# Kernel tuning notes

Measured on AMD Instinct MI355X. Metric: run time of the kernel, lower is better.

Reference implementation:

```python
import jax, jax.numpy as jnp
import numpy as np

N = 20000   # nodes
E = 40000   # edges
B = 1000    # graphs
F = 32      # num_features
D = 64      # dim


def setup_inputs() -> dict:
    key = jax.random.key(0)
    ks = jax.random.split(key, 16)
    def g(k, shape, scale=0.05):
        return jax.random.normal(k, shape, jnp.float32) * scale
    return dict(
        x=jax.random.normal(ks[0], (N, F), jnp.float32),
        edge_attr=jax.random.uniform(ks[1], (E, 5), jnp.float32),
        edge_index=jax.random.randint(ks[2], (2, E), 0, N),
        batch=jnp.sort(jax.random.randint(ks[3], (N,), 0, B)),
        W0=g(ks[4], (D, F)), b0=jnp.zeros((D,), jnp.float32),
        We1=g(ks[5], (128, 5)), be1=jnp.zeros((128,), jnp.float32),
        We2=g(ks[6], (D * D, 128), 0.01), be2=jnp.zeros((D * D,), jnp.float32),
        b_conv=jnp.zeros((D,), jnp.float32),
        W_ih=g(ks[7], (3 * D, D)), W_hh=g(ks[8], (3 * D, D)),
        b_ih=jnp.zeros((3 * D,), jnp.float32), b_hh=jnp.zeros((3 * D,), jnp.float32),
        W_ihl=g(ks[9], (4 * D, 2 * D)), W_hhl=g(ks[10], (4 * D, D)),
        b_ihl=jnp.zeros((4 * D,), jnp.float32), b_hhl=jnp.zeros((4 * D,), jnp.float32),
        W1=g(ks[11], (D, 2 * D)), b1=jnp.zeros((D,), jnp.float32),
        W2=g(ks[12], (1, D)), b2=jnp.zeros((1,), jnp.float32),
    )


def reference(x, edge_attr, edge_index, batch, W0, b0, We1, be1, We2, be2,
              b_conv, W_ih, W_hh, b_ih, b_hh, W_ihl, W_hhl, b_ihl, b_hhl,
              W1, b1, W2, b2):
    src, dst = edge_index[0], edge_index[1]
    # lin0 + relu
    out = jax.nn.relu(x @ W0.T + b0)            # [N, D]
    h = out                                     # GRU hidden
    # edge-conditioned weights (identical each iteration in the original)
    We = jax.nn.relu(edge_attr @ We1.T + be1) @ We2.T + be2
    We = We.reshape(E, D, D)                    # [E, in, out]
    deg = jnp.maximum(jax.ops.segment_sum(jnp.ones((E,), out.dtype), dst, N), 1.0)[:, None]
    for _ in range(3):
        msg = jnp.einsum('ei,eio->eo', out[src], We)          # [E, D]
        agg = jax.ops.segment_sum(msg, dst, num_segments=N) / deg
        m = jax.nn.relu(agg + b_conv)
        # GRU cell (gate order r, z, n as in torch)
        gi = m @ W_ih.T + b_ih
        gh = h @ W_hh.T + b_hh
        ir, iz, inn = jnp.split(gi, 3, -1)
        hr, hz, hn = jnp.split(gh, 3, -1)
        r = jax.nn.sigmoid(ir + hr)
        z = jax.nn.sigmoid(iz + hz)
        n = jnp.tanh(inn + r * hn)
        h = (1.0 - z) * n + z * h
        out = h
    # Set2Set pooling (3 processing steps), LSTM gate order i, f, g, o
    q_star = jnp.zeros((B, 2 * D), out.dtype)
    hl = jnp.zeros((B, D), out.dtype)
    cl = jnp.zeros((B, D), out.dtype)
    for _ in range(3):
        gates = q_star @ W_ihl.T + b_ihl + hl @ W_hhl.T + b_hhl
        i_, f_, g_, o_ = jnp.split(gates, 4, -1)
        cl = jax.nn.sigmoid(f_) * cl + jax.nn.sigmoid(i_) * jnp.tanh(g_)
        hl = jax.nn.sigmoid(o_) * jnp.tanh(cl)
        q = hl                                               # [B, D]
        e = jnp.sum(out * q[batch], -1)                      # [N]
        emax = jax.ops.segment_max(e, batch, num_segments=B)
        a = jnp.exp(e - emax[batch])
        a = a / jax.ops.segment_sum(a, batch, num_segments=B)[batch]
        r_ = jax.ops.segment_sum(a[:, None] * out, batch, num_segments=B)
        q_star = jnp.concatenate([q, r_], -1)                # [B, 2D]
    y = jax.nn.relu(q_star @ W1.T + b1)
    pred = (y @ W2.T + b2).reshape(-1)                       # [B]
    return pred
```

## Files before the change

kernel.cpp:

```cpp
#include <hip/hip_runtime.h>

#define NN 20000
#define NE 40000
#define NGR 1000
#define KH 2
#define WTF_BIAS 524288

typedef unsigned short u16;
typedef u16 u16x8 __attribute__((ext_vector_type(8)));
typedef __bf16 bf16x8 __attribute__((ext_vector_type(8)));
typedef float f32x4 __attribute__((ext_vector_type(4)));

union U8 { u16x8 u; bf16x8 b; };

__device__ __forceinline__ u16 f2bf(float f) {
    union { float f; unsigned u; } v; v.f = f;
    unsigned r = v.u + 0x7FFF + ((v.u >> 16) & 1);
    return (u16)(r >> 16);
}
__device__ __forceinline__ float bf2f(u16 h) {
    union { unsigned u; float f; } v; v.u = ((unsigned)h) << 16;
    return v.f;
}
__device__ __forceinline__ float sigmoidf(float x) { return 1.f / (1.f + __expf(-x)); }

__global__ __launch_bounds__(256) void k_cnt(const int* __restrict__ ei, int* __restrict__ cnt)
{
    for (int e = blockIdx.x * 256 + threadIdx.x; e < NE; e += gridDim.x * 256)
        atomicAdd(&cnt[ei[NE + e]], 1);
}

__global__ __launch_bounds__(1024) void k_scan(const int* __restrict__ cnt,
                                               int* __restrict__ rowptr)
{
    __shared__ int ps[1024];
    int t = threadIdx.x;
    int base = t * 20;
    int loc[20];
    int s = 0;
#pragma unroll
    for (int i = 0; i < 20; ++i) {
        int idx = base + i;
        loc[i] = s;
        s += (idx < NN) ? cnt[idx] : 0;
    }
    ps[t] = s;
    __syncthreads();
    for (int off = 1; off < 1024; off <<= 1) {
        int v = (t >= off) ? ps[t - off] : 0;
        __syncthreads();
        ps[t] += v;
        __syncthreads();
    }
    int ex = (t > 0) ? ps[t - 1] : 0;
#pragma unroll
    for (int i = 0; i < 20; ++i) {
        int idx = base + i;
        if (idx < NN) rowptr[idx] = ex + loc[i];
    }
    if (t == 1023) rowptr[NN] = ps[1023];
}

__global__ __launch_bounds__(256) void k_scatter(const int* __restrict__ ei,
    const int* __restrict__ rowptr, int* __restrict__ cur,
    int* __restrict__ epos, int* __restrict__ srcs)
{
    for (int e = blockIdx.x * 256 + threadIdx.x; e < NE; e += gridDim.x * 256) {
        int d = ei[NE + e];
        int pos = rowptr[d] + atomicAdd(&cur[d], 1);
        epos[e] = pos;
        srcs[pos] = ei[e];
    }
}

__global__ __launch_bounds__(256) void k_pre(
    const float* __restrict__ x, const float* __restrict__ ea,
    const int* __restrict__ batch, const int* __restrict__ epos,
    const float* __restrict__ W0, const float* __restrict__ b0,
    const float* __restrict__ We1, const float* __restrict__ be1,
    const float* __restrict__ We2, const float* __restrict__ be2,
    const float* __restrict__ W_ih, const float* __restrict__ W_hh,
    const float* __restrict__ W_ihl, const float* __restrict__ W_hhl,
    const float* __restrict__ W1,
    float* __restrict__ h, u16* __restrict__ outb, u16* __restrict__ h1,
    u16* __restrict__ WtF, int* __restrict__ gstart, int* __restrict__ gend,
    u16* __restrict__ WgF,
    float* __restrict__ WTihl, float* __restrict__ WThhl, float* __restrict__ WT1)
{
    const int b = blockIdx.x;
    const int t = threadIdx.x;

    if (b < 64) {
        for (int idx = b * 256 + t; idx < 90112; idx += 64 * 256) {
            int i = idx;
            if (i < 32768) {
                int j = i & 7, lane = (i >> 3) & 63;
                int nt = (i >> 9) & 15, ks = i >> 13;
                int o = nt * 16 + (lane & 15);
                int k = ks * 32 + (lane >> 4) * 8 + j;
                float v;
                if (o < 128)      v = (k < 64) ? W_ih[o * 64 + k] : W_hh[o * 64 + k - 64];
                else if (o < 192) v = (k < 64) ? W_ih[o * 64 + k] : 0.f;
                else              v = (k >= 64) ? W_hh[(o - 64) * 64 + k - 64] : 0.f;
                WgF[i] = f2bf(v);
                continue;
            }
            i -= 32768;
            if (i < 32768) { WTihl[i] = W_ihl[(i % 256) * 128 + i / 256]; continue; }
            i -= 32768;
            if (i < 16384) { WThhl[i] = W_hhl[(i % 256) * 64 + i / 256]; continue; }
            i -= 16384;
            WT1[i] = W1[(i % 64) * 128 + i / 64];
        }
        return;
    }
    if (b < 320) {
        int wv = (b - 64) * 4 + (t >> 6);
        int lane = t & 63;
        float w0r[32];
#pragma unroll
        for (int f = 0; f < 32; ++f) w0r[f] = W0[lane * 32 + f];
        float b0v = b0[lane];
        for (int n = wv; n < NN; n += 1024) {
            float xv = (lane < 32) ? x[n * 32 + lane] : 0.f;
            float acc = b0v;
#pragma unroll
            for (int f = 0; f < 32; ++f) acc += __shfl(xv, f, 64) * w0r[f];
            float rv = fmaxf(acc, 0.f);
            h[n * 64 + lane] = rv;
            outb[n * 64 + lane] = f2bf(rv);
        }
        return;
    }
    if (b < 832) {
        for (int idx = (b - 320) * 256 + t; idx < NE * 128; idx += 512 * 256) {
            int e = idx >> 7, k = idx & 127;
            float acc = be1[k];
#pragma unroll
            for (int j = 0; j < 5; ++j)
                acc += ea[e * 5 + j] * We1[k * 5 + j];
            h1[(size_t)epos[e] * 128 + k] = f2bf(fmaxf(acc, 0.f));
        }
        return;
    }
    if (b < 960) {
        for (int idx = (b - 832) * 256 + t; idx < WTF_BIAS + 4096; idx += 128 * 256) {
            float v;
            if (idx < WTF_BIAS) {
                int j = idx & 7, lane = (idx >> 3) & 63;
                int nt = (idx >> 9) & 3, s4 = (idx >> 11) & 3, ch = idx >> 13;
                int o = nt * 16 + (lane & 15);
                int k = s4 * 32 + (lane >> 4) * 8 + j;
                v = We2[(size_t)(ch * 64 + o) * 128 + k];
            } else {
                int bx = idx - WTF_BIAS;
                int j = bx & 7, lane = (bx >> 3) & 63;
                int nt = (bx >> 9) & 3, sb = bx >> 11;
                int o = nt * 16 + (lane & 15);
                int i = sb * 32 + (lane >> 4) * 8 + j;
                v = be2[i * 64 + o];
            }
            WtF[idx] = f2bf(v);
        }
        return;
    }
    {
        for (int idx = (b - 960) * 256 + t; idx < NN; idx += 32 * 256) {
            int bg = batch[idx];
            if (idx == 0 || batch[idx - 1] != bg) gstart[bg] = idx;
            if (idx == NN - 1 || batch[idx + 1] != bg) gend[bg] = idx + 1;
        }
    }
}

__global__ __launch_bounds__(256, 3) void k_msg(
    const u16* __restrict__ outb, const u16* __restrict__ h1,
    const u16* __restrict__ WtF, const int* __restrict__ srcs,
    u16* __restrict__ pbuf)
{
    __shared__ __align__(8) u16 svT[64 * 132];
    const int t = threadIdx.x;
    const int eb0 = blockIdx.x * 128;
    const int kh = blockIdx.y;
    const int ohc = (int)blockIdx.z * 2;

#pragma unroll
    for (int r = 0; r < 4; ++r) {
        int cid = t + 256 * r;
        int row = cid >> 3, c8 = cid & 7;
        int e = eb0 + row;
        u16x8 v = {};
        if (e < NE) { int s = srcs[e]; v = *(const u16x8*)(outb + (size_t)s * 64 + c8 * 8); }
        int rs = row ^ (c8 << 2);
#pragma unroll
        for (int j = 0; j < 8; ++j)
            svT[(c8 * 8 + j) * 132 + rs] = v[j];
    }

    const int lane = t & 63, w = t >> 6, r16 = lane & 15, q = lane >> 4;
    const int w32 = w * 32;

    u16x8 h1r[2][4];
#pragma unroll
    for (int sub = 0; sub < 2; ++sub) {
        int e = eb0 + w32 + sub * 16 + r16;
        if (e >= NE) e = NE - 1;
        const u16* hp = h1 + (size_t)e * 128 + q * 8;
#pragma unroll
        for (int s4 = 0; s4 < 4; ++s4)
            h1r[sub][s4] = *(const u16x8*)(hp + s4 * 32);
    }

    f32x4 acc[2][2];
    const f32x4 z4 = {0.f, 0.f, 0.f, 0.f};
#pragma unroll
    for (int sub = 0; sub < 2; ++sub)
#pragma unroll
        for (int nt = 0; nt < 2; ++nt) acc[sub][nt] = z4;

    f32x4 P0[2][2], P1[2][2];
    U8 bufA[8], bufB[8];
    auto LDC = [&](U8 (&dst)[8], int ch) {
        const u16* p = WtF + (size_t)ch * 8192 + ohc * 512 + lane * 8;
#pragma unroll
        for (int s4 = 0; s4 < 4; ++s4)
#pragma unroll
            for (int nt = 0; nt < 2; ++nt)
                dst[s4 * 2 + nt].u = *(const u16x8*)(p + s4 * 2048 + nt * 512);
    };
    auto MF = [&](f32x4 (&P)[2][2], U8 (&bv)[8]) {
#pragma unroll
        for (int s4 = 0; s4 < 4; ++s4)
#pragma unroll
            for (int sub = 0; sub < 2; ++sub) {
                U8 a; a.u = h1r[sub][s4];
#pragma unroll
                for (int nt = 0; nt < 2; ++nt)
                    P[sub][nt] = __builtin_amdgcn_mfma_f32_16x16x32_bf16(
                        a.b, bv[s4 * 2 + nt].b, (s4 == 0) ? z4 : P[sub][nt], 0, 0, 0);
            }
    };
    auto SCALE = [&](f32x4 (&P)[2][2], int ch) {
        int swz = ((ch >> 3) & 7) << 2;
#pragma unroll
        for (int sub = 0; sub < 2; ++sub) {
            int mb = (w32 + sub * 16 + q * 4) ^ swz;
            uint2 rv = *(const uint2*)&svT[ch * 132 + mb];
            union { unsigned u; float f; } c0, c1, c2, c3;
            c0.u = rv.x << 16; c1.u = rv.x & 0xffff0000u;
            c2.u = rv.y << 16; c3.u = rv.y & 0xffff0000u;
#pragma unroll
            for (int nt = 0; nt < 2; ++nt) {
                acc[sub][nt][0] += c0.f * P[sub][nt][0];
                acc[sub][nt][1] += c1.f * P[sub][nt][1];
                acc[sub][nt][2] += c2.f * P[sub][nt][2];
                acc[sub][nt][3] += c3.f * P[sub][nt][3];
            }
        }
    };

    LDC(bufA, kh * 32);
    __syncthreads();
    LDC(bufB, kh * 32 + 1);
    MF(P0, bufA);

#pragma unroll 1
    for (int cc = 0; cc < 30; cc += 2) {
        const int ch = kh * 32 + cc;
        LDC(bufA, ch + 2);
        MF(P1, bufB);
        SCALE(P0, ch);
        LDC(bufB, ch + 3);
        MF(P0, bufA);
        SCALE(P1, ch + 1);
    }
    MF(P1, bufB);
    SCALE(P0, kh * 32 + 30);
    SCALE(P1, kh * 32 + 31);

    if (kh == KH - 1) {
        U8 bvb[2][2];
#pragma unroll
        for (int sb = 0; sb < 2; ++sb)
#pragma unroll
            for (int nt = 0; nt < 2; ++nt)
                bvb[sb][nt].u = *(const u16x8*)(WtF + WTF_BIAS +
                                                ((sb * 4 + ohc + nt) * 64 + lane) * 8);
#pragma unroll
        for (int sub = 0; sub < 2; ++sub) {
            int m = w32 + sub * 16 + r16;
#pragma unroll
            for (int sb = 0; sb < 2; ++sb) {
                U8 a;
#pragma unroll
                for (int j = 0; j < 8; ++j) {
                    int ch = sb * 32 + q * 8 + j;
                    a.u[j] = svT[ch * 132 + (m ^ (((ch >> 3) & 7) << 2))];
                }
#pragma unroll
                for (int nt = 0; nt < 2; ++nt)
                    acc[sub][nt] = __builtin_amdgcn_mfma_f32_16x16x32_bf16(
                        a.b, bvb[sb][nt].b, acc[sub][nt], 0, 0, 0);
            }
        }
    }

#pragma unroll
    for (int sub = 0; sub < 2; ++sub) {
#pragma unroll
        for (int r = 0; r < 4; ++r) {
            int e = eb0 + w32 + sub * 16 + q * 4 + r;
            if (e >= NE) continue;
            u16* pp = pbuf + (size_t)e * (KH * 64) + kh * 64 + r16;
#pragma unroll
            for (int nt = 0; nt < 2; ++nt)
                pp[(ohc + nt) * 16] = f2bf(acc[sub][nt][r]);
        }
    }
}

__global__ __launch_bounds__(256) void k_gru(float* __restrict__ h, u16* __restrict__ outb,
    const u16* __restrict__ pbuf, const int* __restrict__ rowptr,
    const float* __restrict__ b_conv, const u16* __restrict__ WgF,
    const float* __restrict__ b_ih, const float* __restrict__ b_hh)
{
    __shared__ __align__(16) u16 zA[64 * 132];
    __shared__ float hS[64 * 65];
    const int t = threadIdx.x;
    const int lane = t & 63, w = t >> 6, r16 = lane & 15, q = lane >> 4;
    const int n0 = blockIdx.x * 64;
    const int w16 = w * 16;
    float bcv = b_conv[lane];

#pragma unroll 1
    for (int p = 0; p < 16; ++p) {
        int n = n0 + w16 + p;
        float m = 0.f, hvv = 0.f;
        if (n < NN) {
            int rs = rowptr[n], re = rowptr[n + 1];
            float v = 0.f;
            const u16* pb = pbuf + (size_t)rs * (KH * 64);
            for (int j = rs; j < re; ++j) {
                v += bf2f(pb[lane]) + bf2f(pb[64 + lane]);
                pb += KH * 64;
            }
            m = fmaxf(v / fmaxf((float)(re - rs), 1.f) + bcv, 0.f);
            hvv = h[n * 64 + lane];
        }
        zA[(w16 + p) * 132 + lane] = f2bf(m);
        zA[(w16 + p) * 132 + 64 + lane] = f2bf(hvv);
        hS[(w16 + p) * 65 + lane] = hvv;
    }

    u16x8 afr[4];
#pragma unroll
    for (int ks = 0; ks < 4; ++ks)
        afr[ks] = *(const u16x8*)&zA[(w16 + r16) * 132 + ks * 32 + q * 8];

    f32x4 acc[16];
    const f32x4 z4 = {0.f, 0.f, 0.f, 0.f};
#pragma unroll
    for (int nt = 0; nt < 16; ++nt) acc[nt] = z4;

    U8 bA[4], bB[4];
    auto LDB = [&](U8* dst, int nt) {
#pragma unroll
        for (int ks = 0; ks < 4; ++ks)
            dst[ks].u = *(const u16x8*)(WgF + ((ks * 16 + nt) * 64 + lane) * 8);
    };
    LDB(bA, 0);
#pragma unroll
    for (int nt = 0; nt < 16; ++nt) {
        U8* cur = (nt & 1) ? bB : bA;
        U8* nxt = (nt & 1) ? bA : bB;
        if (nt < 15) LDB(nxt, nt + 1);
        f32x4 c = acc[nt];
#pragma unroll
        for (int ks = 0; ks < 4; ++ks) {
            U8 a; a.u = afr[ks];
            c = __builtin_amdgcn_mfma_f32_16x16x32_bf16(a.b, cur[ks].b, c, 0, 0, 0);
        }
        acc[nt] = c;
    }

#pragma unroll
    for (int reg = 0; reg < 4; ++reg) {
        int nl = w16 + q * 4 + reg;
        int n = n0 + nl;
        if (n >= NN) continue;
#pragma unroll
        for (int dd = 0; dd < 4; ++dd) {
            int d = dd * 16 + r16;
            float rv = acc[dd][reg]      + b_ih[d]       + b_hh[d];
            float zv = acc[4 + dd][reg]  + b_ih[64 + d]  + b_hh[64 + d];
            float iv = acc[8 + dd][reg]  + b_ih[128 + d];
            float hg = acc[12 + dd][reg] + b_hh[128 + d];
            float rr = sigmoidf(rv), zz = sigmoidf(zv);
            float nn = tanhf(iv + rr * hg);
            float hold = hS[nl * 65 + d];
            float hnew = (1.f - zz) * nn + zz * hold;
            h[n * 64 + d] = hnew;
            outb[n * 64 + d] = f2bf(hnew);
        }
    }
}

__global__ __launch_bounds__(256) void k_s2s(const float* __restrict__ h,
    const int* __restrict__ gstart, const int* __restrict__ gend,
    const float* __restrict__ WTihl, const float* __restrict__ WThhl,
    const float* __restrict__ b_ihl, const float* __restrict__ b_hhl,
    const float* __restrict__ WT1, const float* __restrict__ b1,
    const float* __restrict__ W2, const float* __restrict__ b2,
    float* __restrict__ outp)
{
    __shared__ float qs[128];
    __shared__ float hlL[64], clL[64];
    __shared__ float gt[256];
    __shared__ float sm[4], sl[4], sr[4][64];
    const int g = blockIdx.x;
    const int t = threadIdx.x, w = t >> 6, lane = t & 63;
    const int s = gstart[g], e = gend[g];

    if (t < 128) qs[t] = 0.f;
    if (t < 64) { hlL[t] = 0.f; clL[t] = 0.f; }
    __syncthreads();

    for (int step = 0; step < 3; ++step) {
        float ga = b_ihl[t] + b_hhl[t];
#pragma unroll 4
        for (int j = 0; j < 128; ++j)
            ga += qs[j] * WTihl[j * 256 + t];
#pragma unroll 4
        for (int j = 0; j < 64; ++j)
            ga += hlL[j] * WThhl[j * 256 + t];
        gt[t] = ga;
        __syncthreads();
        if (t < 64) {
            float cv = sigmoidf(gt[64 + t]) * clL[t] + sigmoidf(gt[t]) * tanhf(gt[128 + t]);
            float hn = sigmoidf(gt[192 + t]) * tanhf(cv);
            clL[t] = cv; hlL[t] = hn; qs[t] = hn;
        }
        __syncthreads();
        float qv = hlL[lane];
        float M = -3.4e38f, l = 0.f, r = 0.f;
        for (int n = s + w; n < e; n += 4) {
            float hvv = h[n * 64 + lane];
            float p = hvv * qv;
#pragma unroll
            for (int off = 32; off > 0; off >>= 1) p += __shfl_xor(p, off, 64);
            if (p > M) {
                float sc = __expf(M - p);
                l = l * sc + 1.f;
                r = r * sc + hvv;
                M = p;
            } else {
                float pe = __expf(p - M);
                l += pe;
                r += pe * hvv;
            }
        }
        if (lane == 0) { sm[w] = M; sl[w] = l; }
        sr[w][lane] = r;
        __syncthreads();
        if (w == 0) {
            float Mg = fmaxf(fmaxf(sm[0], sm[1]), fmaxf(sm[2], sm[3]));
            float lg = 0.f, rg = 0.f;
#pragma unroll
            for (int wp = 0; wp < 4; ++wp) {
                float sc = __expf(sm[wp] - Mg);
                lg += sl[wp] * sc;
                rg += sr[wp][lane] * sc;
            }
            float inv = (lg > 0.f) ? 1.f / lg : 0.f;
            qs[64 + lane] = rg * inv;
        }
        __syncthreads();
    }
    float acc = 0.f;
#pragma unroll 4
    for (int j = w * 32; j < w * 32 + 32; ++j)
        acc += qs[j] * WT1[j * 64 + lane];
    sr[w][lane] = acc;
    __syncthreads();
    if (w == 0) {
        float y = sr[0][lane] + sr[1][lane] + sr[2][lane] + sr[3][lane] + b1[lane];
        float pr = fmaxf(y, 0.f) * W2[lane];
#pragma unroll
        for (int off = 32; off > 0; off >>= 1) pr += __shfl_xor(pr, off, 64);
        if (lane == 0) outp[g] = pr + b2[0];
    }
}

extern "C" void kernel_launch(void* const* d_in, const int* in_sizes, int n_in,
                              void* d_out, int out_size, void* d_ws, size_t ws_size,
                              hipStream_t stream)
{
    const float* x      = (const float*)d_in[0];
    const float* ea     = (const float*)d_in[1];
    const int*   ei     = (const int*)d_in[2];
    const int*   batch  = (const int*)d_in[3];
    const float* W0     = (const float*)d_in[4];
    const float* b0     = (const float*)d_in[5];
    const float* We1    = (const float*)d_in[6];
    const float* be1    = (const float*)d_in[7];
    const float* We2    = (const float*)d_in[8];
    const float* be2    = (const float*)d_in[9];
    const float* b_conv = (const float*)d_in[10];
    const float* W_ih   = (const float*)d_in[11];
    const float* W_hh   = (const float*)d_in[12];
    const float* b_ih   = (const float*)d_in[13];
    const float* b_hh   = (const float*)d_in[14];
    const float* W_ihl  = (const float*)d_in[15];
    const float* W_hhl  = (const float*)d_in[16];
    const float* b_ihl  = (const float*)d_in[17];
    const float* b_hhl  = (const float*)d_in[18];
    const float* W1     = (const float*)d_in[19];
    const float* b1     = (const float*)d_in[20];
    const float* W2     = (const float*)d_in[21];
    const float* b2     = (const float*)d_in[22];
    float* outp = (float*)d_out;

    char* ws = (char*)d_ws;
    size_t off = 0;
    auto alloc = [&](size_t bytes) -> char* {
        char* p = ws + off;
        off += (bytes + 255) & ~(size_t)255;
        return p;
    };
    u16*   h1     = (u16*)  alloc((size_t)NE * 128 * 2);
    u16*   WtF    = (u16*)  alloc((WTF_BIAS + 4096) * 2);
    u16*   outb   = (u16*)  alloc((size_t)NN * 64 * 2);
    float* h      = (float*)alloc((size_t)NN * 64 * 4);
    u16*   pbuf   = (u16*)  alloc((size_t)NE * KH * 64 * 2);
    int*   rowptr = (int*)  alloc((NN + 1) * 4);
    int*   epos   = (int*)  alloc(NE * 4);
    int*   srcs   = (int*)  alloc(NE * 4);
    int*   cnt    = (int*)  alloc(NN * 4);
    int*   cur    = (int*)  alloc(NN * 4);
    int*   gstart = (int*)  alloc(NGR * 4);
    int*   gend   = (int*)  alloc(NGR * 4);
    u16*   WgF    = (u16*)  alloc(32768 * 2);
    float* WTihl  = (float*)alloc(32768 * 4);
    float* WThhl  = (float*)alloc(16384 * 4);
    float* WT1    = (float*)alloc(8192 * 4);
    if (off > ws_size) return;

    size_t zspan = (size_t)((char*)(gend + NGR) - (char*)cnt);
    hipMemsetAsync(cnt, 0, zspan, stream);

    k_cnt<<<64, 256, 0, stream>>>(ei, cnt);
    k_scan<<<1, 1024, 0, stream>>>(cnt, rowptr);
    k_scatter<<<64, 256, 0, stream>>>(ei, rowptr, cur, epos, srcs);
    k_pre<<<992, 256, 0, stream>>>(x, ea, batch, epos, W0, b0, We1, be1, We2, be2,
                                   W_ih, W_hh, W_ihl, W_hhl, W1,
                                   h, outb, h1, WtF, gstart, gend,
                                   WgF, WTihl, WThhl, WT1);

    dim3 mgrid((NE + 127) / 128, KH, 2);
    for (int it = 0; it < 3; ++it) {
        k_msg<<<mgrid, 256, 0, stream>>>(outb, h1, WtF, srcs, pbuf);
        k_gru<<<313, 256, 0, stream>>>(h, outb, pbuf, rowptr, b_conv,
                                       WgF, b_ih, b_hh);
    }
    k_s2s<<<NGR, 256, 0, stream>>>(h, gstart, gend, WTihl, WThhl, b_ihl, b_hhl,
                                   WT1, b1, W2, b2, outp);
}
```

Measured before the change: 432.9 us.

## Stage per-chunk edge weights into LDS via async global_load_lds double buffer

Replaces per-wave register prefetch of WtF chunks with a cooperative double-buffered LDS staging using global_load_lds, where each wave loads a quarter of the chunk and all waves read it back from LDS. This cuts redundant global/L2 reads of the shared weight tile across the four waves and frees registers, allowing occupancy to be raised from 3 to 4 blocks per CU. It adds two barriers per chunk plus LDS read traffic, uses s_setprio around the MFMA block, and drops the software pipelining that overlapped MFMA with SCALE.

```diff
diff --git a/kernel.cpp b/kernel.cpp
--- a/kernel.cpp
+++ b/kernel.cpp
@@ -23,6 +23,12 @@
     return v.f;
 }
 __device__ __forceinline__ float sigmoidf(float x) { return 1.f / (1.f + __expf(-x)); }
+
+__device__ __forceinline__ void gl_lds16(const u16* g, u16* l) {
+    __builtin_amdgcn_global_load_lds(
+        (const __attribute__((address_space(1))) void*)g,
+        (__attribute__((address_space(3))) void*)l, 16, 0, 0);
+}
 
 __global__ __launch_bounds__(256) void k_cnt(const int* __restrict__ ei, int* __restrict__ cnt)
 {
@@ -173,12 +179,13 @@
     }
 }
 
-__global__ __launch_bounds__(256, 3) void k_msg(
+__global__ __launch_bounds__(256, 4) void k_msg(
     const u16* __restrict__ outb, const u16* __restrict__ h1,
     const u16* __restrict__ WtF, const int* __restrict__ srcs,
     u16* __restrict__ pbuf)
 {
     __shared__ __align__(8) u16 svT[64 * 132];
+    __shared__ __align__(16) u16 LB[2 * 4096];
     const int t = threadIdx.x;
     const int eb0 = blockIdx.x * 128;
     const int kh = blockIdx.y;
@@ -218,27 +225,14 @@
 #pragma unroll
         for (int nt = 0; nt < 2; ++nt) acc[sub][nt] = z4;
 
-    f32x4 P0[2][2], P1[2][2];
-    U8 bufA[8], bufB[8];
-    auto LDC = [&](U8 (&dst)[8], int ch) {
-        const u16* p = WtF + (size_t)ch * 8192 + ohc * 512 + lane * 8;
-#pragma unroll
-        for (int s4 = 0; s4 < 4; ++s4)
-#pragma unroll
-            for (int nt = 0; nt < 2; ++nt)
-                dst[s4 * 2 + nt].u = *(const u16x8*)(p + s4 * 2048 + nt * 512);
-    };
-    auto MF = [&](f32x4 (&P)[2][2], U8 (&bv)[8]) {
-#pragma unroll
-        for (int s4 = 0; s4 < 4; ++s4)
-#pragma unroll
-            for (int sub = 0; sub < 2; ++sub) {
-                U8 a; a.u = h1r[sub][s4];
-#pragma unroll
-                for (int nt = 0; nt < 2; ++nt)
-                    P[sub][nt] = __builtin_amdgcn_mfma_f32_16x16x32_bf16(
-                        a.b, bv[s4 * 2 + nt].b, (s4 == 0) ? z4 : P[sub][nt], 0, 0, 0);
-            }
+    const int chBase = kh * 32;
+    u16* lb0 = &LB[0];
+    u16* lb1 = &LB[4096];
+
+    auto STAGE = [&](u16* lb, int ch) {
+        const u16* g = WtF + (size_t)ch * 8192 + w * 2048 + ohc * 512 + lane * 8;
+        gl_lds16(g,       lb + (2 * w) * 512);
+        gl_lds16(g + 512, lb + (2 * w + 1) * 512);
     };
     auto SCALE = [&](f32x4 (&P)[2][2], int ch) {
         int swz = ((ch >> 3) & 7) << 2;
@@ -259,24 +253,47 @@
         }
     };
 
-    LDC(bufA, kh * 32);
-    __syncthreads();
-    LDC(bufB, kh * 32 + 1);
-    MF(P0, bufA);
+    STAGE(lb0, chBase);
 
 #pragma unroll 1
-    for (int cc = 0; cc < 30; cc += 2) {
-        const int ch = kh * 32 + cc;
-        LDC(bufA, ch + 2);
-        MF(P1, bufB);
-        SCALE(P0, ch);
-        LDC(bufB, ch + 3);
-        MF(P0, bufA);
-        SCALE(P1, ch + 1);
-    }
-    MF(P1, bufB);
-    SCALE(P0, kh * 32 + 30);
-    SCALE(P1, kh * 32 + 31);
+    for (int cc = 0; cc < 32; ++cc) {
+        u16* cur = (cc & 1) ? lb1 : lb0;
+        u16* nxt = (cc & 1) ? lb0 : lb1;
+        if (cc < 31) {
+            STAGE(nxt, chBase + cc + 1);
+            asm volatile("s_waitcnt vmcnt(2) lgkmcnt(0)" ::: "memory");
+        } else {
+            asm volatile("s_waitcnt vmcnt(0) lgkmcnt(0)" ::: "memory");
+        }
+        __builtin_amdgcn_s_barrier();
+        asm volatile("" ::: "memory");
+
+        U8 bv[8];
+#pragma unroll
+        for (int f = 0; f < 8; ++f)
+            bv[f].u = *(const u16x8*)(cur + f * 512 + lane * 8);
+
+        if (cc < 31) {
+            asm volatile("s_waitcnt lgkmcnt(0)" ::: "memory");
+            __builtin_amdgcn_s_barrier();
+            asm volatile("" ::: "memory");
+        }
+
+        __builtin_amdgcn_s_setprio(1);
+        f32x4 P[2][2];
+#pragma unroll
+        for (int s4 = 0; s4 < 4; ++s4)
+#pragma unroll
+            for (int sub = 0; sub < 2; ++sub) {
+                U8 a; a.u = h1r[sub][s4];
+#pragma unroll
+                for (int nt = 0; nt < 2; ++nt)
+                    P[sub][nt] = __builtin_amdgcn_mfma_f32_16x16x32_bf16(
+                        a.b, bv[s4 * 2 + nt].b, (s4 == 0) ? z4 : P[sub][nt], 0, 0, 0);
+            }
+        __builtin_amdgcn_s_setprio(0);
+        SCALE(P, chBase + cc);
+    }
 
     if (kh == KH - 1) {
         U8 bvb[2][2];
```

Result: faster. 423.2 us (-2.3%).
